# Kernel tuning notes

Measured on AMD Instinct MI355X. Metric: run time of the kernel, lower is better.

Reference implementation:

```python
import jax, jax.numpy as jnp
import numpy as np

S = 4096      # total packed sequence length (8 images x 512 patches)
D = 1152      # hidden_dim
H = 16        # num_heads
HD = D // H   # head_dim = 72
MLPD = 4304   # mlp_dim
EPS = 1e-5


def setup_inputs() -> dict:
    key = jax.random.key(0)
    ks = jax.random.split(key, 16)
    f32 = jnp.float32
    w = lambda k, shp: (jax.random.normal(k, shp, f32) * 0.02)
    hidden_states = jax.random.normal(ks[0], (S, D), f32)
    cu_seqlens = (jnp.arange(9, dtype=jnp.int32) * (S // 8))  # [0,512,...,4096]
    angles = jax.random.uniform(ks[1], (S, HD // 2), f32, 0.0, 2.0 * np.pi)
    rope_cos = jnp.cos(angles)
    rope_sin = jnp.sin(angles)
    return {
        "hidden_states": hidden_states,
        "cu_seqlens": cu_seqlens,
        "rope_cos": rope_cos,
        "rope_sin": rope_sin,
        "norm0_scale": jnp.ones((D,), f32),
        "norm0_bias": jnp.zeros((D,), f32),
        "wqkv_w": w(ks[2], (D, 3 * D)),
        "wqkv_b": jnp.zeros((3 * D,), f32),
        "wo_w": w(ks[3], (D, D)),
        "wo_b": jnp.zeros((D,), f32),
        "norm1_scale": jnp.ones((D,), f32),
        "norm1_bias": jnp.zeros((D,), f32),
        "fc0_w": w(ks[4], (D, MLPD)),
        "fc0_b": jnp.zeros((MLPD,), f32),
        "fc1_w": w(ks[5], (MLPD, D)),
        "fc1_b": jnp.zeros((D,), f32),
    }


def _layernorm(x, scale, bias):
    m = jnp.mean(x, axis=-1, keepdims=True)
    v = jnp.mean(jnp.square(x - m), axis=-1, keepdims=True)
    return (x - m) * jax.lax.rsqrt(v + EPS) * scale + bias


def _rope(x, cos, sin):
    # x: (S, H, HD). Complex multiply (x0 + i x1) * (cos + i sin) in real form.
    xr = x.reshape(S, H, HD // 2, 2)
    x0, x1 = xr[..., 0], xr[..., 1]
    c = cos[:, None, :]  # (S, 1, HD/2) broadcast over heads
    s = sin[:, None, :]
    o0 = x0 * c - x1 * s
    o1 = x0 * s + x1 * c
    return jnp.stack([o0, o1], axis=-1).reshape(S, H, HD)


def _block_diag_bias(cu_seqlens):
    positions = jnp.arange(S)
    starts, ends = cu_seqlens[:-1], cu_seqlens[1:]
    in_seg = (positions[:, None] >= starts[None, :]) & (positions[:, None] < ends[None, :])
    seg = jnp.argmax(in_seg.astype(jnp.int32), axis=-1)  # (S,)
    same = seg[:, None] == seg[None, :]
    return jnp.where(same, 0.0, jnp.finfo(jnp.float32).min)  # (S, S)


def reference(hidden_states, cu_seqlens, rope_cos, rope_sin,
              norm0_scale, norm0_bias, wqkv_w, wqkv_b, wo_w, wo_b,
              norm1_scale, norm1_bias, fc0_w, fc0_b, fc1_w, fc1_b):
    # pre-norm attention block
    x = _layernorm(hidden_states, norm0_scale, norm0_bias)
    qkv = (x @ wqkv_w + wqkv_b).reshape(S, 3, H, HD)
    q, k, v = qkv[:, 0], qkv[:, 1], qkv[:, 2]
    q = _rope(q, rope_cos, rope_sin)
    k = _rope(k, rope_cos, rope_sin)
    bias = _block_diag_bias(cu_seqlens)  # (S, S)
    scale = HD ** -0.5
    scores = jnp.einsum('shd,thd->hst', q, k) * scale + bias[None, :, :]
    probs = jax.nn.softmax(scores, axis=-1)
    attn = jnp.einsum('hst,thd->shd', probs, v).reshape(S, D)
    attn = attn @ wo_w + wo_b
    h = hidden_states + attn
    # pre-norm MLP block
    y = _layernorm(h, norm1_scale, norm1_bias)
    y = jax.nn.gelu(y @ fc0_w + fc0_b) @ fc1_w + fc1_b
    return h + y
```

## Files before the change

### kernel.cpp

```cpp
#include <hip/hip_runtime.h>


#define DEV __device__ __forceinline__

typedef __attribute__((ext_vector_type(8))) short short8;
typedef __attribute__((ext_vector_type(4))) float f32x4;

typedef const void __attribute__((address_space(1))) gvoid;
typedef void __attribute__((address_space(3))) lvoid;

DEV ushort f2bf(float f) {
  union { float f; unsigned u; } x; x.f = f;
  unsigned r = (x.u + 0x7FFFu + ((x.u >> 16) & 1u)) >> 16;
  return (ushort)r;
}

DEV float bf2f(ushort u) {
  union { unsigned u; float f; } x; x.u = (unsigned)u << 16;
  return x.f;
}

DEV void gload_lds16(const void* g, void* l) {
  __builtin_amdgcn_global_load_lds((gvoid*)g, (lvoid*)l, 16, 0, 0);
}

DEV f32x4 mfma16(short8 a, short8 b, f32x4 c) {
  return __builtin_amdgcn_mfma_f32_16x16x32_bf16(a, b, c, 0, 0, 0);
}

DEV float gelu_tanh(float x) {
  float x3 = x * x * x;
  return 0.5f * x * (1.f + tanhf(0.7978845608f * (x + 0.044715f * x3)));
}

__global__ void wconv_t(const float* __restrict__ src, ushort* __restrict__ dst,
                        int K, int N, int NP, int KP) {
  __shared__ float tile[32][33];
  const int k0 = blockIdx.x * 32, n0 = blockIdx.y * 32;
  const int tx = threadIdx.x & 31, ty = threadIdx.x >> 5;
#pragma unroll
  for (int i = 0; i < 4; ++i) {
    int r = ty + i * 8;
    float v = 0.f;
    if (k0 + r < K && n0 + tx < N) v = src[(size_t)(k0 + r) * N + n0 + tx];
    tile[tx][r] = v;
  }
  __syncthreads();
#pragma unroll
  for (int i = 0; i < 4; ++i) {
    int r = ty + i * 8;
    dst[(size_t)(n0 + r) * KP + k0 + tx] = f2bf(tile[r][tx]);
  }
}

__global__ __launch_bounds__(256) void ln_bf16(const float* __restrict__ x,
                                               const float* __restrict__ sc,
                                               const float* __restrict__ bi,
                                               ushort* __restrict__ out) {
  const int row = blockIdx.x, tid = threadIdx.x;
  const float* xr = x + (size_t)row * 1152;
  const int n = (tid < 128) ? 5 : 4;
  float vals[5];
  float s = 0.f, s2 = 0.f;
#pragma unroll
  for (int i = 0; i < 5; ++i) {
    if (i < n) { float v = xr[tid + i * 256]; vals[i] = v; s += v; s2 += v * v; }
  }
#pragma unroll
  for (int off = 32; off; off >>= 1) { s += __shfl_xor(s, off); s2 += __shfl_xor(s2, off); }
  __shared__ float rs[4], rs2[4];
  if ((tid & 63) == 0) { rs[tid >> 6] = s; rs2[tid >> 6] = s2; }
  __syncthreads();
  s = rs[0] + rs[1] + rs[2] + rs[3];
  s2 = rs2[0] + rs2[1] + rs2[2] + rs2[3];
  const float mean = s * (1.f / 1152.f);
  const float var = s2 * (1.f / 1152.f) - mean * mean;
  const float rstd = rsqrtf(var + 1e-5f);
  ushort* orow = out + (size_t)row * 1152;
  for (int i = 0; i < n; ++i) {
    int c = tid + i * 256;
    orow[c] = f2bf((vals[i] - mean) * rstd * sc[c] + bi[c]);
  }
}

template <int EPI>
__global__ __launch_bounds__(512, 4) void gemmW(
    const ushort* __restrict__ A, const ushort* __restrict__ Bt,
    const float* __restrict__ bias, const float* __restrict__ resid,
    float* __restrict__ outf, ushort* __restrict__ outh,
    int N, int Kstride, int NT, int n_valid) {
  __shared__ ushort lA[16384];
  __shared__ ushort lB[8192];
  const int tid = threadIdx.x;
  const int lane = tid & 63, wave = tid >> 6;
  const int l15 = lane & 15, lg = lane >> 4;
  const int wm = (wave >> 1) * 64, wn = (wave & 1) * 64;

  const int nx = gridDim.x, ny = gridDim.y;
  const int nwg = nx * ny * gridDim.z;
  const int hw = (blockIdx.z * ny + blockIdx.y) * nx + blockIdx.x;
  const int F = (hw & 7) * (nwg >> 3) + (hw >> 3);
  const int by = F % ny;
  const int C = F / ny;
  const int bx = C % nx;
  const int bz = C / nx;
  const int m0 = by * 256, n0 = bx * 128;
  const int k0 = bz * NT * 64;

  const int swz = ((tid & 7) ^ ((tid >> 3) & 7)) * 8;
  const int rstg = tid >> 3;
  const ushort* Ag = A + (size_t)(m0 + rstg) * Kstride + k0 + swz;
  const ushort* Bg = Bt + (size_t)(n0 + rstg) * Kstride + k0 + swz;

  int offA[4][2], offB[4][2];
#pragma unroll
  for (int f = 0; f < 4; ++f) {
    const int rA = wm + f * 16 + l15;
    const int rB = wn + f * 16 + l15;
#pragma unroll
    for (int ks = 0; ks < 2; ++ks) {
      offA[f][ks] = rA * 64 + (((ks * 4 + lg) ^ (rA & 7))) * 8;
      offB[f][ks] = rB * 64 + (((ks * 4 + lg) ^ (rB & 7))) * 8;
    }
  }

  f32x4 acc[4][4] = {};

  for (int t = 0; t < NT; ++t) {
    const int ko = t * 64;
#pragma unroll
    for (int i = 0; i < 4; ++i)
      gload_lds16(Ag + (size_t)(i * 64) * Kstride + ko, &lA[(i * 512 + tid) * 8]);
#pragma unroll
    for (int i = 0; i < 2; ++i)
      gload_lds16(Bg + (size_t)(i * 64) * Kstride + ko, &lB[(i * 512 + tid) * 8]);
    __syncthreads();
    short8 af[4][2], bfr[4][2];
#pragma unroll
    for (int f = 0; f < 4; ++f) {
#pragma unroll
      for (int ks = 0; ks < 2; ++ks) {
        af[f][ks] = *(const short8*)&lA[offA[f][ks]];
        bfr[f][ks] = *(const short8*)&lB[offB[f][ks]];
      }
    }
#pragma unroll
    for (int i = 0; i < 4; ++i)
#pragma unroll
      for (int j = 0; j < 4; ++j) {
        acc[i][j] = mfma16(af[i][0], bfr[j][0], acc[i][j]);
        acc[i][j] = mfma16(af[i][1], bfr[j][1], acc[i][j]);
      }
    __syncthreads();
  }

  float* outp = outf;
  if constexpr (EPI == 0) outp = outf + (size_t)bz * 4096 * 1152;
  const int cb = n0 + wn + l15;
  const int rb = m0 + wm + lg * 4;
#pragma unroll
  for (int j = 0; j < 4; ++j) {
    const int col = cb + j * 16;
    const float bv = (EPI != 0 && col < n_valid) ? bias[col] : 0.f;
#pragma unroll
    for (int i = 0; i < 4; ++i) {
#pragma unroll
      for (int r = 0; r < 4; ++r) {
        const int row = rb + i * 16 + r;
        const size_t idx = (size_t)row * N + col;
        const float v = acc[i][j][r] + bv;
        if constexpr (EPI == 0) outp[idx] = v;
        else if constexpr (EPI == 1) outf[idx] = resid[idx] + v;
        else if constexpr (EPI == 2) outh[idx] = f2bf(gelu_tanh(v));
        else outh[idx] = f2bf(v);
      }
    }
  }
}

template <int EPI>
__global__ __launch_bounds__(256, 3) void gemmS(
    const ushort* __restrict__ A, const ushort* __restrict__ Bt,
    const float* __restrict__ bias, const float* __restrict__ resid,
    float* __restrict__ outf, ushort* __restrict__ outh,
    int N, int Kstride, int NT, int n_valid) {
  __shared__ ushort lA[8192];
  __shared__ ushort lB[8192];
  const int tid = threadIdx.x;
  const int lane = tid & 63, wave = tid >> 6;
  const int l15 = lane & 15, lg = lane >> 4;
  const int wm = (wave >> 1) * 64, wn = (wave & 1) * 64;

  const int nx = gridDim.x, ny = gridDim.y;
  const int nwg = nx * ny * gridDim.z;
  const int hw = (blockIdx.z * ny + blockIdx.y) * nx + blockIdx.x;
  const int F = (hw & 7) * (nwg >> 3) + (hw >> 3);
  const int by = F % ny;
  const int C = F / ny;
  const int bx = C % nx;
  const int bz = C / nx;
  const int m0 = by * 128, n0 = bx * 128;
  const int k0 = bz * NT * 64;

  const int swz = ((tid & 7) ^ ((tid >> 3) & 7)) * 8;
  const int rstg = tid >> 3;
  const ushort* Ag = A + (size_t)(m0 + rstg) * Kstride + k0 + swz;
  const ushort* Bg = Bt + (size_t)(n0 + rstg) * Kstride + k0 + swz;

  int offA[4][2], offB[4][2];
#pragma unroll
  for (int f = 0; f < 4; ++f) {
    const int rA = wm + f * 16 + l15;
    const int rB = wn + f * 16 + l15;
#pragma unroll
    for (int ks = 0; ks < 2; ++ks) {
      offA[f][ks] = rA * 64 + (((ks * 4 + lg) ^ (rA & 7))) * 8;
      offB[f][ks] = rB * 64 + (((ks * 4 + lg) ^ (rB & 7))) * 8;
    }
  }

  f32x4 acc[4][4] = {};

  for (int t = 0; t < NT; ++t) {
    const int ko = t * 64;
#pragma unroll
    for (int i = 0; i < 4; ++i)
      gload_lds16(Ag + (size_t)(i * 32) * Kstride + ko, &lA[(i * 256 + tid) * 8]);
#pragma unroll
    for (int i = 0; i < 4; ++i)
      gload_lds16(Bg + (size_t)(i * 32) * Kstride + ko, &lB[(i * 256 + tid) * 8]);
    __syncthreads();
    short8 af[4][2], bfr[4][2];
#pragma unroll
    for (int f = 0; f < 4; ++f) {
#pragma unroll
      for (int ks = 0; ks < 2; ++ks) {
        af[f][ks] = *(const short8*)&lA[offA[f][ks]];
        bfr[f][ks] = *(const short8*)&lB[offB[f][ks]];
      }
    }
#pragma unroll
    for (int i = 0; i < 4; ++i)
#pragma unroll
      for (int j = 0; j < 4; ++j) {
        acc[i][j] = mfma16(af[i][0], bfr[j][0], acc[i][j]);
        acc[i][j] = mfma16(af[i][1], bfr[j][1], acc[i][j]);
      }
    __syncthreads();
  }

  float* outp = outf;
  if constexpr (EPI == 0) outp = outf + (size_t)bz * 4096 * 1152;
  const int cb = n0 + wn + l15;
  const int rb = m0 + wm + lg * 4;
#pragma unroll
  for (int j = 0; j < 4; ++j) {
    const int col = cb + j * 16;
    const float bv = (EPI != 0 && col < n_valid) ? bias[col] : 0.f;
#pragma unroll
    for (int i = 0; i < 4; ++i) {
#pragma unroll
      for (int r = 0; r < 4; ++r) {
        const int row = rb + i * 16 + r;
        const size_t idx = (size_t)row * N + col;
        const float v = acc[i][j][r] + bv;
        if constexpr (EPI == 0) outp[idx] = v;
        else if constexpr (EPI == 1) outf[idx] = resid[idx] + v;
        else if constexpr (EPI == 2) outh[idx] = f2bf(gelu_tanh(v));
        else outh[idx] = f2bf(v);
      }
    }
  }
}

__global__ __launch_bounds__(256) void ksum_reduce(
    const float* __restrict__ hb, const float* __restrict__ bias,
    const float* __restrict__ p0, const float* __restrict__ p1,
    float* __restrict__ out) {
  const f32x4* hb4 = (const f32x4*)hb;
  const f32x4* b4 = (const f32x4*)bias;
  const f32x4* p04 = (const f32x4*)p0;
  const f32x4* p14 = (const f32x4*)p1;
  f32x4* o4 = (f32x4*)out;
  const int total = 4096 * 288;
  for (int i = blockIdx.x * 256 + threadIdx.x; i < total; i += gridDim.x * 256)
    o4[i] = hb4[i] + b4[i % 288] + p04[i] + p14[i];
}

__global__ __launch_bounds__(256) void rope_pack(
    const ushort* __restrict__ qkv,
    const float* __restrict__ cosp, const float* __restrict__ sinp,
    ushort* __restrict__ qp, ushort* __restrict__ kp) {
  const int t = blockIdx.x * 256 + threadIdx.x;
  const int c = t % 12;
  const int hs = t / 12;
  const int h = hs & 15;
  const int s = hs >> 4;
  const size_t dst = ((size_t)h * 4096 + s) * 96 + c * 8;
  if (c >= 9) {
    short8 z = {};
    *(short8*)(qp + dst) = z;
    *(short8*)(kp + dst) = z;
    return;
  }
  const size_t base = (size_t)s * 3456 + h * 72 + c * 8;
  const short8 qv = *(const short8*)(qkv + base);
  const short8 kv = *(const short8*)(qkv + base + 1152);
  const f32x4 cs = *(const f32x4*)(cosp + s * 36 + c * 4);
  const f32x4 sn = *(const f32x4*)(sinp + s * 36 + c * 4);
  short8 qo, ko;
#pragma unroll
  for (int j = 0; j < 4; ++j) {
    const float q0 = bf2f((ushort)qv[2 * j]), q1 = bf2f((ushort)qv[2 * j + 1]);
    const float k0 = bf2f((ushort)kv[2 * j]), k1 = bf2f((ushort)kv[2 * j + 1]);
    qo[2 * j] = (short)f2bf((q0 * cs[j] - q1 * sn[j]) * 0.1178511302f);
    qo[2 * j + 1] = (short)f2bf((q0 * sn[j] + q1 * cs[j]) * 0.1178511302f);
    ko[2 * j] = (short)f2bf(k0 * cs[j] - k1 * sn[j]);
    ko[2 * j + 1] = (short)f2bf(k0 * sn[j] + k1 * cs[j]);
  }
  *(short8*)(qp + dst) = qo;
  *(short8*)(kp + dst) = ko;
}

__global__ void v_pack(const ushort* __restrict__ qkv, ushort* __restrict__ vt) {
  __shared__ ushort lv[96][64];
  const int b = blockIdx.x;
  const int h = b >> 6;
  const int s0 = (b & 63) << 6;
  const int tid = threadIdx.x;
#pragma unroll
  for (int it = 0; it < 24; ++it) {
    int idx = tid + it * 256;
    int d = idx % 96, sl = idx / 96;
    lv[d][sl] = (d < 72) ? qkv[(size_t)(s0 + sl) * 3456 + 2304 + h * 72 + d] : (ushort)0;
  }
  __syncthreads();
#pragma unroll
  for (int it = 0; it < 24; ++it) {
    int idx = tid + it * 256;
    int d = idx >> 6, sl = idx & 63;
    vt[((size_t)h * 96 + d) * 4096 + s0 + sl] = lv[d][sl];
  }
}

__global__ __launch_bounds__(256) void attn_kernel(
    const ushort* __restrict__ qp, const ushort* __restrict__ kp,
    const ushort* __restrict__ vt, ushort* __restrict__ attn_out) {
  __shared__ ushort lp[4][16 * 32];
  const int tid = threadIdx.x, lane = tid & 63, wave = tid >> 6;
  const int l15 = lane & 15, lg = lane >> 4;
  const int b = blockIdx.x;
  const int h = b >> 6;
  const int rem = b & 63;
  const int seg = rem >> 3, qt = rem & 7;
  const int q0 = seg * 512 + qt * 64 + wave * 16;

  short8 aq[3];
  const ushort* qrow = qp + ((size_t)h * 4096 + q0 + l15) * 96 + lg * 8;
  aq[0] = *(const short8*)(qrow);
  aq[1] = *(const short8*)(qrow + 32);
  aq[2] = *(const short8*)(qrow + 64);

  f32x4 oacc[5] = {};
  float mrow[4] = {-1e30f, -1e30f, -1e30f, -1e30f};
  float srow[4] = {0.f, 0.f, 0.f, 0.f};

  const ushort* kbase = kp + ((size_t)h * 4096 + seg * 512) * 96;
  const ushort* vbase = vt + (size_t)h * 96 * 4096 + seg * 512;
  ushort* lpw = lp[wave];

  for (int kc = 0; kc < 16; ++kc) {
    f32x4 sc[2] = {};
#pragma unroll
    for (int n = 0; n < 2; ++n) {
      const ushort* krow = kbase + (size_t)(kc * 32 + n * 16 + l15) * 96 + lg * 8;
#pragma unroll
      for (int c = 0; c < 3; ++c) {
        short8 kb = *(const short8*)(krow + c * 32);
        sc[n] = mfma16(aq[c], kb, sc[n]);
      }
    }
    float corr[4];
#pragma unroll
    for (int j = 0; j < 4; ++j) {
      float v = fmaxf(sc[0][j], sc[1][j]);
      v = fmaxf(v, __shfl_xor(v, 1));
      v = fmaxf(v, __shfl_xor(v, 2));
      v = fmaxf(v, __shfl_xor(v, 4));
      v = fmaxf(v, __shfl_xor(v, 8));
      float mn = fmaxf(mrow[j], v);
      corr[j] = __expf(mrow[j] - mn);
      mrow[j] = mn;
    }
    float p0[4], p1[4];
#pragma unroll
    for (int j = 0; j < 4; ++j) {
      p0[j] = __expf(sc[0][j] - mrow[j]);
      p1[j] = __expf(sc[1][j] - mrow[j]);
      float ps = p0[j] + p1[j];
      ps += __shfl_xor(ps, 1);
      ps += __shfl_xor(ps, 2);
      ps += __shfl_xor(ps, 4);
      ps += __shfl_xor(ps, 8);
      srow[j] = srow[j] * corr[j] + ps;
    }
#pragma unroll
    for (int n = 0; n < 5; ++n)
#pragma unroll
      for (int j = 0; j < 4; ++j)
        oacc[n][j] *= corr[j];
#pragma unroll
    for (int j = 0; j < 4; ++j) {
      int row = lg * 4 + j;
      lpw[row * 32 + l15] = f2bf(p0[j]);
      lpw[row * 32 + 16 + l15] = f2bf(p1[j]);
    }
    __syncthreads();
    short8 pa = *(const short8*)&lpw[l15 * 32 + lg * 8];
    const ushort* vrow = vbase + kc * 32 + lg * 8;
#pragma unroll
    for (int n = 0; n < 5; ++n) {
      short8 vb = *(const short8*)(vrow + (size_t)(n * 16 + l15) * 4096);
      oacc[n] = mfma16(pa, vb, oacc[n]);
    }
    __syncthreads();
  }
#pragma unroll
  for (int j = 0; j < 4; ++j) {
    float inv = 1.f / srow[j];
    int row = q0 + lg * 4 + j;
#pragma unroll
    for (int n = 0; n < 5; ++n) {
      int col = n * 16 + l15;
      if (col < 72)
        attn_out[(size_t)row * 1152 + h * 72 + col] = f2bf(oacc[n][j] * inv);
    }
  }
}

extern "C" void kernel_launch(void* const* d_in, const int* in_sizes, int n_in,
                              void* d_out, int out_size, void* d_ws, size_t ws_size,
                              hipStream_t stream) {
  (void)in_sizes; (void)n_in; (void)out_size;
  const float* hidden = (const float*)d_in[0];
  const float* ropec = (const float*)d_in[2];
  const float* ropes = (const float*)d_in[3];
  const float* n0s = (const float*)d_in[4];
  const float* n0b = (const float*)d_in[5];
  const float* wqkv = (const float*)d_in[6];
  const float* bqkv = (const float*)d_in[7];
  const float* wo = (const float*)d_in[8];
  const float* bo = (const float*)d_in[9];
  const float* n1s = (const float*)d_in[10];
  const float* n1b = (const float*)d_in[11];
  const float* wfc0 = (const float*)d_in[12];
  const float* bfc0 = (const float*)d_in[13];
  const float* wfc1 = (const float*)d_in[14];
  const float* bfc1 = (const float*)d_in[15];
  float* out = (float*)d_out;

  char* ws = (char*)d_ws;
  ushort* x_bf   = (ushort*)(ws + 0);
  ushort* wqkv_t = (ushort*)(ws + 9437184);
  ushort* wo_t   = (ushort*)(ws + 17399808);
  ushort* fc0_t  = (ushort*)(ws + 20054016);
  ushort* fc1_t  = (ushort*)(ws + 30081024);
  ushort* qkv_bf = (ushort*)(ws + 40108032);
  ushort* mid    = (ushort*)(ws + 40108032);
  ushort* q_pad  = (ushort*)(ws + 75759616);
  ushort* k_pad  = (ushort*)(ws + 88342528);
  ushort* vt     = (ushort*)(ws + 100925440);
  float*  pbuf   = (float*)(ws + 75759616);
  ushort* attn   = (ushort*)(ws + 113508352);
  float*  hbuf   = (float*)(ws + 122945536);
  ushort* yln    = (ushort*)(ws + 141819904);
  if (ws_size < 151257088) return;

  wconv_t<<<dim3(36, 108), 256, 0, stream>>>(wqkv, wqkv_t, 1152, 3456, 3456, 1152);
  wconv_t<<<dim3(36, 36), 256, 0, stream>>>(wo, wo_t, 1152, 1152, 1152, 1152);
  wconv_t<<<dim3(36, 136), 256, 0, stream>>>(wfc0, fc0_t, 1152, 4304, 4352, 1152);
  wconv_t<<<dim3(136, 36), 256, 0, stream>>>(wfc1, fc1_t, 4304, 1152, 1152, 4352);

  ln_bf16<<<4096, 256, 0, stream>>>(hidden, n0s, n0b, x_bf);

  gemmW<3><<<dim3(27, 16), 512, 0, stream>>>(x_bf, wqkv_t, bqkv, nullptr, nullptr, qkv_bf,
                                             3456, 1152, 18, 3456);
  rope_pack<<<3072, 256, 0, stream>>>(qkv_bf, ropec, ropes, q_pad, k_pad);
  v_pack<<<1024, 256, 0, stream>>>(qkv_bf, vt);

  attn_kernel<<<1024, 256, 0, stream>>>(q_pad, k_pad, vt, attn);

  gemmS<1><<<dim3(9, 32), 256, 0, stream>>>(attn, wo_t, bo, hidden, hbuf, nullptr,
                                            1152, 1152, 18, 1152);
  ln_bf16<<<4096, 256, 0, stream>>>(hbuf, n1s, n1b, yln);

  gemmW<2><<<dim3(34, 16), 512, 0, stream>>>(yln, fc0_t, bfc0, nullptr, nullptr, mid,
                                             4352, 1152, 18, 4304);
  gemmS<0><<<dim3(9, 32, 2), 256, 0, stream>>>(mid, fc1_t, nullptr, nullptr, pbuf, nullptr,
                                               1152, 4352, 34, 1152);
  ksum_reduce<<<2048, 256, 0, stream>>>(hbuf, bfc1, pbuf, pbuf + (size_t)4096 * 1152, out);
}
```

Baseline: 338.1 us.

## Add 256x256 ping-pong pipelined GEMM kernel for QKV projection

Adds a new gemmT kernel with 256x256 tiles, double-buffered LDS, direct global-to-LDS loads and a fine-grained interleaved schedule. That schedule uses barriers, explicit waitcnt and setprio to overlap MFMA work with the next tile's loads. The QKV projection is switched to this kernel with a 14x16 grid, and the transposed QKV weight is padded to 3584 columns so whole 256-wide tiles fit. Larger tiles raise data reuse per workgroup but cut the number of workgroups (224 on a 256-CU part) and raise register and LDS pressure.

```diff
diff --git a/kernel.cpp b/kernel.cpp
--- a/kernel.cpp
+++ b/kernel.cpp
@@ -80,6 +80,147 @@
   for (int i = 0; i < n; ++i) {
     int c = tid + i * 256;
     orow[c] = f2bf((vals[i] - mean) * rstd * sc[c] + bi[c]);
+  }
+}
+
+#define BAR __builtin_amdgcn_s_barrier()
+#define LGKM0 do { asm volatile("s_waitcnt lgkmcnt(0)" ::: "memory"); \
+                   __builtin_amdgcn_sched_barrier(0); } while (0)
+#define VM6 do { asm volatile("s_waitcnt vmcnt(6)" ::: "memory"); \
+                 __builtin_amdgcn_sched_barrier(0); } while (0)
+#define MMQ(AF, BF, MB, NB)                                                   \
+  do {                                                                        \
+    __builtin_amdgcn_s_setprio(1);                                            \
+    _Pragma("unroll") for (int mf = 0; mf < 4; ++mf)                          \
+      _Pragma("unroll") for (int nf = 0; nf < 2; ++nf) {                      \
+        acc[(MB) + mf][(NB) + nf] =                                           \
+            mfma16(AF[mf][0], BF[nf][0], acc[(MB) + mf][(NB) + nf]);          \
+        acc[(MB) + mf][(NB) + nf] =                                           \
+            mfma16(AF[mf][1], BF[nf][1], acc[(MB) + mf][(NB) + nf]);          \
+      }                                                                       \
+    __builtin_amdgcn_s_setprio(0);                                            \
+  } while (0)
+
+template <int EPI>
+__global__ __launch_bounds__(512, 2) void gemmT(
+    const ushort* __restrict__ A, const ushort* __restrict__ Bt,
+    const float* __restrict__ bias, const float* __restrict__ resid,
+    float* __restrict__ outf, ushort* __restrict__ outh,
+    int N, int K, int NT, int n_valid) {
+  __shared__ ushort lA[2][256 * 64];
+  __shared__ ushort lB[2][256 * 64];
+  const int tid = threadIdx.x;
+  const int lane = tid & 63, wave = tid >> 6;
+  const int l15 = lane & 15, lg = lane >> 4;
+  const int wr = wave >> 2, wc = wave & 3;
+
+  const int nx = gridDim.x, ny = gridDim.y;
+  const int nwg = nx * ny * gridDim.z;
+  int flat = (blockIdx.z * ny + blockIdx.y) * nx + blockIdx.x;
+  flat = (flat & 7) * (nwg >> 3) + (flat >> 3);
+  const int bx = flat % nx;
+  const int rem = flat / nx;
+  const int by = rem % ny;
+  const int bz = rem / ny;
+  const int m0 = by * 256, n0 = bx * 256;
+  const int k0 = bz * NT * 64;
+
+  const int rb8 = tid >> 3;
+  const int swz = ((tid & 7) ^ (rb8 & 7)) * 8;
+  const ushort* Ag = A + (size_t)m0 * K + k0 + swz;
+  const ushort* Bg = Bt + (size_t)n0 * K + k0 + swz;
+  const int rB = (rb8 & 31) + ((rb8 >> 5) << 6);
+  const int rBw = (wave & 3) * 8 + (wave >> 2) * 64;
+
+  auto stA = [&](int b, int u, int t) {
+#pragma unroll
+    for (int j = 0; j < 2; ++j) {
+      const int r = u * 64 + rb8 + j * 128;
+      gload_lds16(Ag + (size_t)r * K + t * 64,
+                  &lA[b][(u * 64 + wave * 8 + j * 128) * 64]);
+    }
+  };
+  auto stB = [&](int b, int c, int t) {
+#pragma unroll
+    for (int j = 0; j < 2; ++j) {
+      const int r = rB + c * 32 + j * 128;
+      gload_lds16(Bg + (size_t)r * K + t * 64,
+                  &lB[b][(rBw + c * 32 + j * 128) * 64]);
+    }
+  };
+
+  const int arow = wr * 128 + l15;
+  const int brow = wc * 64 + l15;
+  const int cp0 = ((0 + lg) ^ (l15 & 7)) * 8;
+  const int cp1 = ((4 + lg) ^ (l15 & 7)) * 8;
+  auto rdA = [&](int b, int half, short8 (&a)[4][2]) {
+#pragma unroll
+    for (int mf = 0; mf < 4; ++mf) {
+      const ushort* p = &lA[b][(arow + half * 64 + mf * 16) * 64];
+      a[mf][0] = *(const short8*)(p + cp0);
+      a[mf][1] = *(const short8*)(p + cp1);
+    }
+  };
+  auto rdB = [&](int b, int h, short8 (&bb)[2][2]) {
+#pragma unroll
+    for (int nf = 0; nf < 2; ++nf) {
+      const ushort* p = &lB[b][(brow + h * 32 + nf * 16) * 64];
+      bb[nf][0] = *(const short8*)(p + cp0);
+      bb[nf][1] = *(const short8*)(p + cp1);
+    }
+  };
+
+  f32x4 acc[8][4] = {};
+  short8 aL[4][2], aH[4][2], b01[2][2], b23[2][2];
+
+  stA(0, 0, 0); stB(0, 0, 0); stA(0, 1, 0); stB(0, 1, 0);
+  stA(1, 0, 1); stB(1, 0, 1); stA(1, 1, 1); stB(1, 1, 1);
+  asm volatile("s_waitcnt vmcnt(8)" ::: "memory");
+  BAR;
+  rdA(0, 0, aL); rdB(0, 0, b01);
+
+  const int NIT = NT >> 1;
+  for (int it = 0; it < NIT; ++it) {
+    const int tn0 = 2 * it + 2, tn1 = 2 * it + 3;
+    const bool more = (it + 1 < NIT);
+    rdB(0, 1, b23); if (more) stA(0, 0, tn0);
+    BAR; LGKM0; MMQ(aL, b01, 0, 0); BAR;
+    rdA(0, 1, aH); if (more) stB(0, 0, tn0);
+    BAR; LGKM0; MMQ(aL, b23, 0, 2); BAR;
+    if (more) stA(0, 1, tn0);
+    BAR; LGKM0; MMQ(aH, b01, 4, 0); VM6; BAR;
+    rdA(1, 0, aL); rdB(1, 0, b01); if (more) stB(0, 1, tn0);
+    BAR; LGKM0; MMQ(aH, b23, 4, 2); BAR;
+    rdB(1, 1, b23); if (more) stA(1, 0, tn1);
+    BAR; LGKM0; MMQ(aL, b01, 0, 0); BAR;
+    rdA(1, 1, aH); if (more) stB(1, 0, tn1);
+    BAR; LGKM0; MMQ(aL, b23, 0, 2); BAR;
+    if (more) stA(1, 1, tn1);
+    BAR; LGKM0; MMQ(aH, b01, 4, 0); VM6; BAR;
+    rdA(0, 0, aL); rdB(0, 0, b01); if (more) stB(1, 1, tn1);
+    BAR; LGKM0; MMQ(aH, b23, 4, 2); BAR;
+  }
+
+  float* outp = outf;
+  if constexpr (EPI == 0) outp = outf + (size_t)bz * 4096 * 1152;
+#pragma unroll
+  for (int nf = 0; nf < 4; ++nf) {
+    const int col = n0 + wc * 64 + nf * 16 + l15;
+    if (col >= n_valid) continue;
+    const float bv = (EPI != 0) ? bias[col] : 0.f;
+#pragma unroll
+    for (int mf = 0; mf < 8; ++mf) {
+#pragma unroll
+      for (int r = 0; r < 4; ++r) {
+        const int row = m0 + wr * 128 + mf * 16 + lg * 4 + r;
+        const size_t idx = (size_t)row * N + col;
+        const float v = acc[mf][nf][r] + bv;
+        if constexpr (EPI == 0) outp[idx] = v;
+        else if constexpr (EPI == 1) outf[idx] = resid[idx] + v;
+        else if constexpr (EPI == 2) outh[idx] = f2bf(gelu_tanh(v));
+        else outh[idx] = f2bf(v);
+      }
+    }
   }
 }
 
@@ -462,28 +603,28 @@
   char* ws = (char*)d_ws;
   ushort* x_bf   = (ushort*)(ws + 0);
   ushort* wqkv_t = (ushort*)(ws + 9437184);
-  ushort* wo_t   = (ushort*)(ws + 17399808);
-  ushort* fc0_t  = (ushort*)(ws + 20054016);
-  ushort* fc1_t  = (ushort*)(ws + 30081024);
-  ushort* qkv_bf = (ushort*)(ws + 40108032);
-  ushort* mid    = (ushort*)(ws + 40108032);
-  ushort* q_pad  = (ushort*)(ws + 75759616);
-  ushort* k_pad  = (ushort*)(ws + 88342528);
-  ushort* vt     = (ushort*)(ws + 100925440);
-  float*  pbuf   = (float*)(ws + 75759616);
-  ushort* attn   = (ushort*)(ws + 113508352);
-  float*  hbuf   = (float*)(ws + 122945536);
-  ushort* yln    = (ushort*)(ws + 141819904);
-  if (ws_size < 151257088) return;
-
-  wconv_t<<<dim3(36, 108), 256, 0, stream>>>(wqkv, wqkv_t, 1152, 3456, 3456, 1152);
+  ushort* wo_t   = (ushort*)(ws + 17694720);
+  ushort* fc0_t  = (ushort*)(ws + 20348928);
+  ushort* fc1_t  = (ushort*)(ws + 30375936);
+  ushort* qkv_bf = (ushort*)(ws + 40402944);
+  ushort* mid    = (ushort*)(ws + 40402944);
+  ushort* q_pad  = (ushort*)(ws + 76054528);
+  ushort* k_pad  = (ushort*)(ws + 88637440);
+  ushort* vt     = (ushort*)(ws + 101220352);
+  float*  pbuf   = (float*)(ws + 76054528);
+  ushort* attn   = (ushort*)(ws + 113803264);
+  float*  hbuf   = (float*)(ws + 123240448);
+  ushort* yln    = (ushort*)(ws + 142114816);
+  if (ws_size < 151552000) return;
+
+  wconv_t<<<dim3(36, 112), 256, 0, stream>>>(wqkv, wqkv_t, 1152, 3456, 3584, 1152);
   wconv_t<<<dim3(36, 36), 256, 0, stream>>>(wo, wo_t, 1152, 1152, 1152, 1152);
   wconv_t<<<dim3(36, 136), 256, 0, stream>>>(wfc0, fc0_t, 1152, 4304, 4352, 1152);
   wconv_t<<<dim3(136, 36), 256, 0, stream>>>(wfc1, fc1_t, 4304, 1152, 1152, 4352);
 
   ln_bf16<<<4096, 256, 0, stream>>>(hidden, n0s, n0b, x_bf);
 
-  gemmW<3><<<dim3(27, 16), 512, 0, stream>>>(x_bf, wqkv_t, bqkv, nullptr, nullptr, qkv_bf,
+  gemmT<3><<<dim3(14, 16), 512, 0, stream>>>(x_bf, wqkv_t, bqkv, nullptr, nullptr, qkv_bf,
                                              3456, 1152, 18, 3456);
   rope_pack<<<3072, 256, 0, stream>>>(qkv_bf, ropec, ropes, q_pad, k_pad);
   v_pack<<<1024, 256, 0, stream>>>(qkv_bf, vt);
```

Result: slower. 351.2 us (+3.9%).
